# Kernel optimization log

Measured on AMD Instinct MI355X. Metric: run time of the kernel, lower is better.

Reference implementation:

```python
import jax, jax.numpy as jnp
import numpy as np

D_MODEL = 1024
NUM_HEADS = 16
DEPTH = D_MODEL // NUM_HEADS


def setup_inputs() -> dict:
    key = jax.random.key(0)
    ks = jax.random.split(key, 9)
    B, S = 2, 2048
    s = 1.0 / np.sqrt(D_MODEL)
    return {
        "x": jax.random.normal(ks[0], (B, S, D_MODEL), dtype=jnp.float32),
        "wq": jax.random.normal(ks[1], (D_MODEL, D_MODEL), dtype=jnp.float32) * s,
        "bq": jnp.zeros((D_MODEL,), dtype=jnp.float32),
        "wk": jax.random.normal(ks[2], (D_MODEL, D_MODEL), dtype=jnp.float32) * s,
        "bk": jnp.zeros((D_MODEL,), dtype=jnp.float32),
        "wv": jax.random.normal(ks[3], (D_MODEL, D_MODEL), dtype=jnp.float32) * s,
        "bv": jnp.zeros((D_MODEL,), dtype=jnp.float32),
        "wo": jax.random.normal(ks[4], (D_MODEL, D_MODEL), dtype=jnp.float32) * s,
        "bo": jnp.zeros((D_MODEL,), dtype=jnp.float32),
    }


def _split_heads(t):
    # [B, S, D] -> [B, H, S, depth]
    B, S, _ = t.shape
    return t.reshape(B, S, NUM_HEADS, DEPTH).transpose(0, 2, 1, 3)


def reference(x, wq, bq, wk, bk, wv, bv, wo, bo):
    B, S, _ = x.shape
    q = _split_heads(x @ wq + bq)
    k = _split_heads(x @ wk + bk)
    v = _split_heads(x @ wv + bv)
    scale = 1.0 / jnp.sqrt(jnp.asarray(DEPTH, dtype=x.dtype))
    logits = jnp.einsum("bhsd,bhtd->bhst", q, k) * scale  # [B,H,S,S]
    attn = jax.nn.softmax(logits, axis=-1)
    ctx = jnp.einsum("bhst,bhtd->bhsd", attn, v)  # [B,H,S,depth]
    concat = ctx.transpose(0, 2, 1, 3).reshape(B, S, D_MODEL)
    return concat @ wo + bo
```

## Files before the change

### kernel.cpp

```cpp
#include <hip/hip_runtime.h>
#include <hip/hip_bf16.h>

typedef __bf16 bf16;
typedef __bf16 bf16x4 __attribute__((ext_vector_type(4)));
typedef __bf16 bf16x8 __attribute__((ext_vector_type(8)));
typedef float f32x4 __attribute__((ext_vector_type(4)));

typedef __attribute__((address_space(3))) void lds_void;
typedef const __attribute__((address_space(1))) void gbl_void;

#define D_MODEL 1024
#define NHEAD 16
#define DEPTH 64
#define SEQ 2048
#define BATCH 2
#define NTOK (BATCH * SEQ)

#define Q_SCALE 0.18033688f

__global__ __launch_bounds__(256) void prep(const float* __restrict__ w0,
                                            const float* __restrict__ w1,
                                            const float* __restrict__ w2,
                                            const float* __restrict__ w3,
                                            const float* __restrict__ x,
                                            bf16* __restrict__ wtb,
                                            bf16* __restrict__ xb) {
    int z = blockIdx.z;
    int tx = threadIdx.x, ty = threadIdx.y;
    if (z < 4) {
        const float* w = (z == 0) ? w0 : (z == 1) ? w1 : (z == 2) ? w2 : w3;
        bf16* d = wtb + (size_t)z * D_MODEL * D_MODEL;
        __shared__ float tile[32][33];
        int c0 = blockIdx.x * 32;
        int r0 = blockIdx.y * 32;
#pragma unroll
        for (int i = 0; i < 4; i++)
            tile[ty + i * 8][tx] = w[(size_t)(r0 + ty + i * 8) * D_MODEL + c0 + tx];
        __syncthreads();
#pragma unroll
        for (int i = 0; i < 4; i++)
            d[(size_t)(c0 + ty + i * 8) * D_MODEL + r0 + tx] = (bf16)tile[tx][ty + i * 8];
    } else {
        int t = ty * 32 + tx;
        size_t i = ((size_t)(z - 4) * 1024 + blockIdx.y * 32 + blockIdx.x) * 256 + t;
        float4 v = ((const float4*)x)[i];
        bf16x4 o = {(bf16)v.x, (bf16)v.y, (bf16)v.z, (bf16)v.w};
        *(bf16x4*)&xb[i * 4] = o;
    }
}

__global__ __launch_bounds__(512, 2) void qkv_gemm(const bf16* __restrict__ xb,
                                                   const bf16* __restrict__ wtb,
                                                   const float* __restrict__ bq,
                                                   const float* __restrict__ bk,
                                                   const float* __restrict__ bv,
                                                   bf16* __restrict__ q,
                                                   bf16* __restrict__ k,
                                                   bf16* __restrict__ v) {
    __shared__ bf16 sm[65536];

    const int flat = blockIdx.x;
    const int wg = (flat & 7) * 24 + (flat >> 3);
    const int mt = wg & 15, nt = wg >> 4;
    const int row0 = mt << 8;
    const int z = nt >> 2;
    const int nb = (nt & 3) << 8;

    const int tid = threadIdx.x;
    const int lane = tid & 63, wave = tid >> 6;
    const int wm = wave >> 2, wn = wave & 3;
    const int quad = lane >> 4, l16 = lane & 15;
    const int kch = ((quad ^ ((l16 >> 1) & 3)) << 3);

    const int srow = lane >> 2;
    const int scg = (lane & 3) ^ ((lane >> 3) & 3);
    const int stDst = wave * 1024 + lane * 8;

    const bf16* Ag = xb + (size_t)(row0 + wave * 32 + srow) * D_MODEL + scg * 8;
    const bf16* Bg = wtb + (size_t)z * D_MODEL * D_MODEL
                   + (size_t)(nb + wave * 32 + srow) * D_MODEL + scg * 8;

    f32x4 acc[8][4] = {};
    bf16x8 bfr[4];

#define GLL(SRC, DST) __builtin_amdgcn_global_load_lds((gbl_void*)(SRC), (lds_void*)(DST), 16, 0, 0)
#define STG_A(T_, KQ_, BUF_) { \
    const bf16* s_ = Ag + (T_) * 64 + (KQ_) * 32; \
    bf16* d_ = sm + (BUF_) * 16384 + (KQ_) * 8192 + stDst; \
    GLL(s_, d_); GLL(s_ + 16 * D_MODEL, d_ + 512); }
#define STG_B(T_, KQ_, BUF_) { \
    const bf16* s_ = Bg + (T_) * 64 + (KQ_) * 32; \
    bf16* d_ = sm + 32768 + (BUF_) * 16384 + (KQ_) * 8192 + stDst; \
    GLL(s_, d_); GLL(s_ + 16 * D_MODEL, d_ + 512); }
#define WAIT6 { asm volatile("s_waitcnt vmcnt(6)" ::: "memory"); }
#define NOW

#define PHASE(BUF_, KQ_, MQ_, STG_STMT, WAIT_STMT) { \
    bf16x8 af[4]; \
    const int ab_ = (BUF_) * 16384 + (KQ_) * 8192 + (wm * 128 + (MQ_) * 64 + l16) * 32 + kch; \
    _Pragma("unroll") \
    for (int i_ = 0; i_ < 4; i_++) af[i_] = *(const bf16x8*)&sm[ab_ + i_ * 512]; \
    if ((MQ_) == 0) { \
        const int bb_ = 32768 + (BUF_) * 16384 + (KQ_) * 8192 + (wn * 64 + l16) * 32 + kch; \
        _Pragma("unroll") \
        for (int j_ = 0; j_ < 4; j_++) bfr[j_] = *(const bf16x8*)&sm[bb_ + j_ * 512]; \
    } \
    STG_STMT; \
    WAIT_STMT; \
    __builtin_amdgcn_sched_barrier(0); \
    __builtin_amdgcn_s_barrier(); \
    __builtin_amdgcn_s_setprio(1); \
    _Pragma("unroll") \
    for (int i_ = 0; i_ < 4; i_++) \
        _Pragma("unroll") \
        for (int j_ = 0; j_ < 4; j_++) \
            acc[(MQ_) * 4 + i_][j_] = __builtin_amdgcn_mfma_f32_16x16x32_bf16( \
                af[i_], bfr[j_], acc[(MQ_) * 4 + i_][j_], 0, 0, 0); \
    __builtin_amdgcn_s_setprio(0); \
    __builtin_amdgcn_sched_barrier(0); \
    __builtin_amdgcn_s_barrier(); }

    STG_B(0, 0, 0);
    STG_A(0, 0, 0);
    STG_B(0, 1, 0);
    STG_A(0, 1, 0);
    asm volatile("s_waitcnt vmcnt(4)" ::: "memory");
    STG_B(1, 0, 1);
    STG_A(1, 0, 1);
    STG_B(1, 1, 1);
    asm volatile("s_waitcnt vmcnt(6)" ::: "memory");
    __builtin_amdgcn_sched_barrier(0);
    __builtin_amdgcn_s_barrier();

#pragma unroll 1
    for (int it = 0; it < 8; ++it) {
        const int t1 = 2 * it + 1;
        const int t2 = (2 * it + 2) & 15;
        const int t3 = (2 * it + 3) & 15;
        PHASE(0, 0, 0, STG_A(t1, 1, 1), NOW)
        PHASE(0, 0, 1, STG_B(t2, 0, 0), NOW)
        PHASE(0, 1, 0, STG_A(t2, 0, 0), NOW)
        PHASE(0, 1, 1, STG_B(t2, 1, 0), WAIT6)
        PHASE(1, 0, 0, STG_A(t2, 1, 0), NOW)
        PHASE(1, 0, 1, STG_B(t3, 0, 1), NOW)
        PHASE(1, 1, 0, STG_A(t3, 0, 1), NOW)
        PHASE(1, 1, 1, STG_B(t3, 1, 1), WAIT6)
    }

#undef PHASE
#undef WAIT6
#undef NOW
#undef STG_A
#undef STG_B
#undef GLL

    const float* bias = (z == 0) ? bq : (z == 1) ? bk : bv;
    const int bI = row0 >> 11;
    const int sBase = row0 & 2047;
    if (z < 2) {
        bf16* dst = (z == 0) ? q : k;
        const float scl = (z == 0) ? Q_SCALE : 1.0f;
#pragma unroll
        for (int j = 0; j < 4; j++) {
            const int f = nb + wn * 64 + j * 16 + l16;
            const float bi = bias[f];
            const int hh = f >> 6, d = f & 63;
            bf16* dcol = dst + ((size_t)(bI * NHEAD + hh) * SEQ) * DEPTH + d;
#pragma unroll
            for (int mi = 0; mi < 8; mi++) {
                const int s0 = sBase + wm * 128 + (mi >> 2) * 64 + (mi & 3) * 16 + quad * 4;
#pragma unroll
                for (int r = 0; r < 4; r++)
                    dcol[(size_t)(s0 + r) * DEPTH] = (bf16)((acc[mi][j][r] + bi) * scl);
            }
        }
    } else {
#pragma unroll
        for (int j = 0; j < 4; j++) {
            const int f = nb + wn * 64 + j * 16 + l16;
            const float bi = bias[f];
            const int hh = f >> 6, d = f & 63;
            bf16* vrow = v + ((size_t)(bI * NHEAD + hh) * DEPTH + d) * SEQ;
#pragma unroll
            for (int mi = 0; mi < 8; mi++) {
                const int s0 = sBase + wm * 128 + (mi >> 2) * 64 + (mi & 3) * 16 + quad * 4;
                f32x4 a = acc[mi][j];
                bf16x4 ob = {(bf16)(a[0] + bi), (bf16)(a[1] + bi),
                             (bf16)(a[2] + bi), (bf16)(a[3] + bi)};
                *(bf16x4*)&vrow[s0] = ob;
            }
        }
    }
}

__global__ __launch_bounds__(256) void attn(const bf16* __restrict__ q,
                                            const bf16* __restrict__ k,
                                            const bf16* __restrict__ v,
                                            bf16* __restrict__ ctx) {
    __shared__ __align__(16) bf16 smb[32768];
    const int tid = threadIdx.x;
    const int lane = tid & 63, wave = tid >> 6;
    const int quad = lane >> 4, l16 = lane & 15;
    const int bh = blockIdx.x;
    const int q0 = blockIdx.y * 64;
    const size_t hb = (size_t)bh * SEQ * DEPTH;
    const bf16* qh = q + hb;
    const bf16* kh = k + hb;
    const bf16* vh = v + hb;

    bf16x8 bq_[4][2];
#pragma unroll
    for (int n = 0; n < 4; n++) {
        int qrow = q0 + n * 16 + l16;
#pragma unroll
        for (int c = 0; c < 2; c++)
            bq_[n][c] = *(const bf16x8*)&qh[(size_t)qrow * DEPTH + c * 32 + quad * 8];
    }

    f32x4 ov[4][4] = {};
    f32x4 lv = {};

    const int wb = wave * 8192;
    const int kchS = (lane & 7) ^ (((lane >> 3) & 3) << 1);
    const int vchS = (lane & 3) ^ ((lane >> 2) & 3);
    const int krdL = ((l16 >> 2) << 3) + (l16 & 3);
    const int ksw = ((l16 & 3) << 1) | ((l16 >> 2) & 1);
    const int vsw = (quad ^ (l16 & 3)) << 3;

#define GLL(SRC, DST) __builtin_amdgcn_global_load_lds((gbl_void*)(SRC), (lds_void*)(DST), 16, 0, 0)

#define STAGE(BUF_, T_) { \
    _Pragma("unroll") \
    for (int o_ = 0; o_ < 4; o_++) { \
        const bf16* s_ = kh + (size_t)((T_) + wave * 32 + o_ * 8 + (lane >> 3)) * DEPTH \
                       + ((kchS ^ (o_ & 1)) << 3); \
        GLL(s_, smb + wb + (BUF_) * 2048 + o_ * 512 + lane * 8); \
    } \
    _Pragma("unroll") \
    for (int o_ = 0; o_ < 4; o_++) { \
        const bf16* s_ = vh + (size_t)(o_ * 16 + (lane >> 2)) * SEQ + (T_) + wave * 32 \
                       + (vchS << 3); \
        GLL(s_, smb + wb + 4096 + (BUF_) * 2048 + o_ * 512 + lane * 8); \
    } }

#define COMPUTE(BUF_) { \
    f32x4 s[2][4] = {}; \
    __builtin_amdgcn_s_setprio(1); \
    _Pragma("unroll") \
    for (int c_ = 0; c_ < 2; c_++) \
        _Pragma("unroll") \
        for (int h_ = 0; h_ < 2; h_++) { \
            bf16x8 kf = *(const bf16x8*)&smb[wb + (BUF_) * 2048 + (krdL + h_ * 4) * 64 \
                                             + ((((c_ << 2) | quad) ^ ksw) << 3)]; \
            _Pragma("unroll") \
            for (int n_ = 0; n_ < 4; n_++) \
                s[h_][n_] = __builtin_amdgcn_mfma_f32_16x16x32_bf16(kf, bq_[n_][c_], s[h_][n_], 0, 0, 0); \
        } \
    __builtin_amdgcn_s_setprio(0); \
    bf16x8 pb[4]; \
    _Pragma("unroll") \
    for (int n_ = 0; n_ < 4; n_++) { \
        float e0 = __builtin_amdgcn_exp2f(s[0][n_][0]); \
        float e1 = __builtin_amdgcn_exp2f(s[0][n_][1]); \
        float e2 = __builtin_amdgcn_exp2f(s[0][n_][2]); \
        float e3 = __builtin_amdgcn_exp2f(s[0][n_][3]); \
        float e4 = __builtin_amdgcn_exp2f(s[1][n_][0]); \
        float e5 = __builtin_amdgcn_exp2f(s[1][n_][1]); \
        float e6 = __builtin_amdgcn_exp2f(s[1][n_][2]); \
        float e7 = __builtin_amdgcn_exp2f(s[1][n_][3]); \
        pb[n_][0] = (bf16)e0; pb[n_][1] = (bf16)e1; \
        pb[n_][2] = (bf16)e2; pb[n_][3] = (bf16)e3; \
        pb[n_][4] = (bf16)e4; pb[n_][5] = (bf16)e5; \
        pb[n_][6] = (bf16)e6; pb[n_][7] = (bf16)e7; \
        lv[n_] += ((e0 + e1) + (e2 + e3)) + ((e4 + e5) + (e6 + e7)); \
    } \
    __builtin_amdgcn_s_setprio(1); \
    _Pragma("unroll") \
    for (int t_ = 0; t_ < 4; t_++) { \
        bf16x8 vf = *(const bf16x8*)&smb[wb + 4096 + (BUF_) * 2048 + (t_ * 16 + l16) * 32 + vsw]; \
        _Pragma("unroll") \
        for (int n_ = 0; n_ < 4; n_++) \
            ov[t_][n_] = __builtin_amdgcn_mfma_f32_16x16x32_bf16(vf, pb[n_], ov[t_][n_], 0, 0, 0); \
    } \
    __builtin_amdgcn_s_setprio(0); }

#define WAITV(N_) { asm volatile("s_waitcnt vmcnt(" #N_ ")" ::: "memory"); }
#define SB0 __builtin_amdgcn_sched_barrier(0)

    const int tb = wave << 2;
    STAGE(0, ((tb) & 15) * 128);
#pragma unroll 1
    for (int i = 0; i < 16; i++) {
        if (i < 15) {
            STAGE((i + 1) & 1, ((tb + i + 1) & 15) * 128);
            WAITV(8);
        } else {
            WAITV(0);
        }
        SB0;
        COMPUTE(i & 1);
        SB0;
    }

#undef SB0
#undef WAITV
#undef COMPUTE
#undef STAGE
#undef GLL

    f32x4* Red  = (f32x4*)smb;
    f32x4* Lred = (f32x4*)((char*)smb + 32768);
    __syncthreads();
#pragma unroll
    for (int tt = 0; tt < 8; tt++)
        Red[(tt * 4 + wave) * 64 + lane] = ov[tt >> 2][tt & 3];
    Lred[wave * 64 + lane] = lv;
    __syncthreads();
    f32x4 ls = {};
#pragma unroll
    for (int w_ = 0; w_ < 4; w_++)
#pragma unroll
        for (int qd = 0; qd < 4; qd++)
            ls += Lred[w_ * 64 + qd * 16 + l16];
    const int b = bh >> 4, hh = bh & 15;
    const int wb1 = wave & 1;
#pragma unroll
    for (int u = 0; u < 2; u++) {
        int tt = wave * 2 + u;
        f32x4 sv = Red[(tt * 4 + 0) * 64 + lane] + Red[(tt * 4 + 1) * 64 + lane]
                 + Red[(tt * 4 + 2) * 64 + lane] + Red[(tt * 4 + 3) * 64 + lane];
        int n = wb1 * 2 + u, t = wave >> 1;
        float iv = 1.0f / (wb1 ? ls[2 + u] : ls[u]);
        bf16x4 ob = {(bf16)(sv[0] * iv), (bf16)(sv[1] * iv),
                     (bf16)(sv[2] * iv), (bf16)(sv[3] * iv)};
        size_t off = ((size_t)(b * SEQ + q0 + n * 16 + l16)) * D_MODEL
                   + hh * 64 + t * 16 + quad * 4;
        *(bf16x4*)&ctx[off] = ob;
    }
    __syncthreads();
#pragma unroll
    for (int tt = 8; tt < 16; tt++)
        Red[((tt - 8) * 4 + wave) * 64 + lane] = ov[tt >> 2][tt & 3];
    __syncthreads();
#pragma unroll
    for (int u = 0; u < 2; u++) {
        int rt = wave * 2 + u;
        f32x4 sv = Red[(rt * 4 + 0) * 64 + lane] + Red[(rt * 4 + 1) * 64 + lane]
                 + Red[(rt * 4 + 2) * 64 + lane] + Red[(rt * 4 + 3) * 64 + lane];
        int n = wb1 * 2 + u, t = 2 + (wave >> 1);
        float iv = 1.0f / (wb1 ? ls[2 + u] : ls[u]);
        bf16x4 ob = {(bf16)(sv[0] * iv), (bf16)(sv[1] * iv),
                     (bf16)(sv[2] * iv), (bf16)(sv[3] * iv)};
        size_t off = ((size_t)(b * SEQ + q0 + n * 16 + l16)) * D_MODEL
                   + hh * 64 + t * 16 + quad * 4;
        *(bf16x4*)&ctx[off] = ob;
    }
}

__global__ __launch_bounds__(256) void out_gemm(const bf16* __restrict__ ctx,
                                                const bf16* __restrict__ wot,
                                                const float* __restrict__ bo,
                                                float* __restrict__ out) {
    __shared__ bf16 As[64 * 32];
    __shared__ bf16 Bs[128 * 32];
    const int tid = threadIdx.x;
    const int lane = tid & 63, wave = tid >> 6;
    const int quad = lane >> 4, l16 = lane & 15;
    const int srow = lane >> 2, selem = (lane & 3) * 8;
    int row0 = blockIdx.y * 64, col0 = blockIdx.x * 128;
    f32x4 acc[4][2] = {};

    for (int k0 = 0; k0 < D_MODEL; k0 += 32) {
        __syncthreads();
        {
            const bf16* ga = ctx + (size_t)(row0 + wave * 16 + srow) * D_MODEL + k0 + selem;
            __builtin_amdgcn_global_load_lds((gbl_void*)ga, (lds_void*)(As + wave * 512 + lane * 8), 16, 0, 0);
        }
#pragma unroll
        for (int t = 0; t < 2; t++) {
            int m = wave * 2 + t;
            const bf16* gb = wot + (size_t)(col0 + m * 16 + srow) * D_MODEL + k0 + selem;
            __builtin_amdgcn_global_load_lds((gbl_void*)gb, (lds_void*)(Bs + m * 512 + lane * 8), 16, 0, 0);
        }
        __syncthreads();
        bf16x8 af[4], bfr[2];
#pragma unroll
        for (int i = 0; i < 4; i++)
            af[i] = *(const bf16x8*)&As[(i * 16 + l16) * 32 + quad * 8];
#pragma unroll
        for (int j = 0; j < 2; j++)
            bfr[j] = *(const bf16x8*)&Bs[(wave * 32 + j * 16 + l16) * 32 + quad * 8];
#pragma unroll
        for (int i = 0; i < 4; i++)
#pragma unroll
            for (int j = 0; j < 2; j++)
                acc[i][j] = __builtin_amdgcn_mfma_f32_16x16x32_bf16(af[i], bfr[j], acc[i][j], 0, 0, 0);
    }
#pragma unroll
    for (int i = 0; i < 4; i++)
#pragma unroll
        for (int j = 0; j < 2; j++) {
            int colg = col0 + wave * 32 + j * 16 + l16;
            float bi = bo[colg];
            int rbase = row0 + i * 16 + quad * 4;
#pragma unroll
            for (int r = 0; r < 4; r++)
                out[(size_t)(rbase + r) * D_MODEL + colg] = acc[i][j][r] + bi;
        }
}

extern "C" void kernel_launch(void* const* d_in, const int* in_sizes, int n_in,
                              void* d_out, int out_size, void* d_ws, size_t ws_size,
                              hipStream_t stream) {
    const float* x  = (const float*)d_in[0];
    const float* wq = (const float*)d_in[1];
    const float* bq = (const float*)d_in[2];
    const float* wk = (const float*)d_in[3];
    const float* bk = (const float*)d_in[4];
    const float* wv = (const float*)d_in[5];
    const float* bv = (const float*)d_in[6];
    const float* wo = (const float*)d_in[7];
    const float* bo = (const float*)d_in[8];
    float* out = (float*)d_out;

    const size_t MB = 1024 * 1024;
    char* ws = (char*)d_ws;
    bf16* xb  = (bf16*)(ws);
    bf16* wtb = (bf16*)(ws + 8 * MB);
    bf16* qb  = (bf16*)(ws + 16 * MB);
    bf16* kb  = (bf16*)(ws + 24 * MB);
    bf16* vb  = (bf16*)(ws + 32 * MB);
    bf16* ctx = (bf16*)(ws + 40 * MB);

    prep<<<dim3(32, 32, 8), dim3(32, 8), 0, stream>>>(wq, wk, wv, wo, x, wtb, xb);
    qkv_gemm<<<dim3(192), dim3(512), 0, stream>>>(xb, wtb, bq, bk, bv, qb, kb, vb);
    attn<<<dim3(BATCH * NHEAD, SEQ / 64), 256, 0, stream>>>(qb, kb, vb, ctx);
    out_gemm<<<dim3(8, 64), 256, 0, stream>>>(ctx, wtb + 3 * (size_t)D_MODEL * D_MODEL, bo, out);
}
```

Before: 191.1 us.

## Split attention block into 8 waves sharing K/V tiles across query groups

The attention kernel now launches 512 threads per block. Waves are split into 4 key-split groups times 2 query groups of 32 rows each. Only the first query group issues the global-to-LDS loads of K/V tiles, and both groups read the shared tiles, with block-wide barriers added around each compute step. The intent is more waves per CU and fewer accumulator registers per wave, which should improve latency hiding. The cost is two s_barriers per iteration and all waves walking through the K tiles in lockstep instead of staggered.

```diff
diff --git a/kernel.cpp b/kernel.cpp
--- a/kernel.cpp
+++ b/kernel.cpp
@@ -193,13 +193,14 @@
     }
 }
 
-__global__ __launch_bounds__(256) void attn(const bf16* __restrict__ q,
-                                            const bf16* __restrict__ k,
-                                            const bf16* __restrict__ v,
-                                            bf16* __restrict__ ctx) {
+__global__ __launch_bounds__(512, 4) void attn(const bf16* __restrict__ q,
+                                               const bf16* __restrict__ k,
+                                               const bf16* __restrict__ v,
+                                               bf16* __restrict__ ctx) {
     __shared__ __align__(16) bf16 smb[32768];
     const int tid = threadIdx.x;
     const int lane = tid & 63, wave = tid >> 6;
+    const int ks = wave & 3, qg = wave >> 2;
     const int quad = lane >> 4, l16 = lane & 15;
     const int bh = blockIdx.x;
     const int q0 = blockIdx.y * 64;
@@ -208,19 +209,19 @@
     const bf16* kh = k + hb;
     const bf16* vh = v + hb;
 
-    bf16x8 bq_[4][2];
-#pragma unroll
-    for (int n = 0; n < 4; n++) {
-        int qrow = q0 + n * 16 + l16;
+    bf16x8 bq_[2][2];
+#pragma unroll
+    for (int n = 0; n < 2; n++) {
+        int qrow = q0 + qg * 32 + n * 16 + l16;
 #pragma unroll
         for (int c = 0; c < 2; c++)
             bq_[n][c] = *(const bf16x8*)&qh[(size_t)qrow * DEPTH + c * 32 + quad * 8];
     }
 
-    f32x4 ov[4][4] = {};
-    f32x4 lv = {};
-
-    const int wb = wave * 8192;
+    f32x4 ov[4][2] = {};
+    float lvs[2] = {0.f, 0.f};
+
+    const int sb = ks * 8192;
     const int kchS = (lane & 7) ^ (((lane >> 3) & 3) << 1);
     const int vchS = (lane & 3) ^ ((lane >> 2) & 3);
     const int krdL = ((l16 >> 2) << 3) + (l16 & 3);
@@ -232,34 +233,34 @@
 #define STAGE(BUF_, T_) { \
     _Pragma("unroll") \
     for (int o_ = 0; o_ < 4; o_++) { \
-        const bf16* s_ = kh + (size_t)((T_) + wave * 32 + o_ * 8 + (lane >> 3)) * DEPTH \
+        const bf16* s_ = kh + (size_t)((T_) + ks * 32 + o_ * 8 + (lane >> 3)) * DEPTH \
                        + ((kchS ^ (o_ & 1)) << 3); \
-        GLL(s_, smb + wb + (BUF_) * 2048 + o_ * 512 + lane * 8); \
+        GLL(s_, smb + sb + (BUF_) * 2048 + o_ * 512 + lane * 8); \
     } \
     _Pragma("unroll") \
     for (int o_ = 0; o_ < 4; o_++) { \
-        const bf16* s_ = vh + (size_t)(o_ * 16 + (lane >> 2)) * SEQ + (T_) + wave * 32 \
+        const bf16* s_ = vh + (size_t)(o_ * 16 + (lane >> 2)) * SEQ + (T_) + ks * 32 \
                        + (vchS << 3); \
-        GLL(s_, smb + wb + 4096 + (BUF_) * 2048 + o_ * 512 + lane * 8); \
+        GLL(s_, smb + sb + 4096 + (BUF_) * 2048 + o_ * 512 + lane * 8); \
     } }
 
 #define COMPUTE(BUF_) { \
-    f32x4 s[2][4] = {}; \
+    f32x4 s[2][2] = {}; \
     __builtin_amdgcn_s_setprio(1); \
     _Pragma("unroll") \
     for (int c_ = 0; c_ < 2; c_++) \
         _Pragma("unroll") \
         for (int h_ = 0; h_ < 2; h_++) { \
-            bf16x8 kf = *(const bf16x8*)&smb[wb + (BUF_) * 2048 + (krdL + h_ * 4) * 64 \
+            bf16x8 kf = *(const bf16x8*)&smb[sb + (BUF_) * 2048 + (krdL + h_ * 4) * 64 \
                                              + ((((c_ << 2) | quad) ^ ksw) << 3)]; \
             _Pragma("unroll") \
-            for (int n_ = 0; n_ < 4; n_++) \
+            for (int n_ = 0; n_ < 2; n_++) \
                 s[h_][n_] = __builtin_amdgcn_mfma_f32_16x16x32_bf16(kf, bq_[n_][c_], s[h_][n_], 0, 0, 0); \
         } \
     __builtin_amdgcn_s_setprio(0); \
-    bf16x8 pb[4]; \
-    _Pragma("unroll") \
-    for (int n_ = 0; n_ < 4; n_++) { \
+    bf16x8 pb[2]; \
+    _Pragma("unroll") \
+    for (int n_ = 0; n_ < 2; n_++) { \
         float e0 = __builtin_amdgcn_exp2f(s[0][n_][0]); \
         float e1 = __builtin_amdgcn_exp2f(s[0][n_][1]); \
         float e2 = __builtin_amdgcn_exp2f(s[0][n_][2]); \
@@ -272,87 +273,97 @@
         pb[n_][2] = (bf16)e2; pb[n_][3] = (bf16)e3; \
         pb[n_][4] = (bf16)e4; pb[n_][5] = (bf16)e5; \
         pb[n_][6] = (bf16)e6; pb[n_][7] = (bf16)e7; \
-        lv[n_] += ((e0 + e1) + (e2 + e3)) + ((e4 + e5) + (e6 + e7)); \
+        lvs[n_] += ((e0 + e1) + (e2 + e3)) + ((e4 + e5) + (e6 + e7)); \
     } \
     __builtin_amdgcn_s_setprio(1); \
     _Pragma("unroll") \
     for (int t_ = 0; t_ < 4; t_++) { \
-        bf16x8 vf = *(const bf16x8*)&smb[wb + 4096 + (BUF_) * 2048 + (t_ * 16 + l16) * 32 + vsw]; \
+        bf16x8 vf = *(const bf16x8*)&smb[sb + 4096 + (BUF_) * 2048 + (t_ * 16 + l16) * 32 + vsw]; \
         _Pragma("unroll") \
-        for (int n_ = 0; n_ < 4; n_++) \
+        for (int n_ = 0; n_ < 2; n_++) \
             ov[t_][n_] = __builtin_amdgcn_mfma_f32_16x16x32_bf16(vf, pb[n_], ov[t_][n_], 0, 0, 0); \
     } \
     __builtin_amdgcn_s_setprio(0); }
 
-#define WAITV(N_) { asm volatile("s_waitcnt vmcnt(" #N_ ")" ::: "memory"); }
 #define SB0 __builtin_amdgcn_sched_barrier(0)
 
-    const int tb = wave << 2;
-    STAGE(0, ((tb) & 15) * 128);
+    if (qg == 0) STAGE(0, 0);
 #pragma unroll 1
     for (int i = 0; i < 16; i++) {
-        if (i < 15) {
-            STAGE((i + 1) & 1, ((tb + i + 1) & 15) * 128);
-            WAITV(8);
-        } else {
-            WAITV(0);
+        if (qg == 0) {
+            if (i < 15) {
+                STAGE((i + 1) & 1, (i + 1) * 128);
+                asm volatile("s_waitcnt vmcnt(8)" ::: "memory");
+            } else {
+                asm volatile("s_waitcnt vmcnt(0)" ::: "memory");
+            }
         }
         SB0;
+        __builtin_amdgcn_s_barrier();
         COMPUTE(i & 1);
         SB0;
+        __builtin_amdgcn_s_barrier();
     }
 
 #undef SB0
-#undef WAITV
 #undef COMPUTE
 #undef STAGE
 #undef GLL
 
     f32x4* Red  = (f32x4*)smb;
-    f32x4* Lred = (f32x4*)((char*)smb + 32768);
+    float* Lred = (float*)((char*)smb + 32768);
+    const int b = bh >> 4, hh = bh & 15;
+    const int tA = ks >> 1, nA = ks & 1;
+
     __syncthreads();
 #pragma unroll
-    for (int tt = 0; tt < 8; tt++)
-        Red[(tt * 4 + wave) * 64 + lane] = ov[tt >> 2][tt & 3];
-    Lred[wave * 64 + lane] = lv;
+    for (int t2 = 0; t2 < 2; t2++)
+#pragma unroll
+        for (int n = 0; n < 2; n++)
+            Red[((((qg * 2 + t2) * 2 + n) * 4) + ks) * 64 + lane] = ov[t2][n];
+#pragma unroll
+    for (int n = 0; n < 2; n++)
+        Lred[((qg * 2 + n) * 4 + ks) * 64 + lane] = lvs[n];
     __syncthreads();
-    f32x4 ls = {};
-#pragma unroll
-    for (int w_ = 0; w_ < 4; w_++)
-#pragma unroll
-        for (int qd = 0; qd < 4; qd++)
-            ls += Lred[w_ * 64 + qd * 16 + l16];
-    const int b = bh >> 4, hh = bh & 15;
-    const int wb1 = wave & 1;
-#pragma unroll
-    for (int u = 0; u < 2; u++) {
-        int tt = wave * 2 + u;
-        f32x4 sv = Red[(tt * 4 + 0) * 64 + lane] + Red[(tt * 4 + 1) * 64 + lane]
-                 + Red[(tt * 4 + 2) * 64 + lane] + Red[(tt * 4 + 3) * 64 + lane];
-        int n = wb1 * 2 + u, t = wave >> 1;
-        float iv = 1.0f / (wb1 ? ls[2 + u] : ls[u]);
+
+    float ls0 = 0.f, ls1 = 0.f;
+#pragma unroll
+    for (int k4 = 0; k4 < 4; k4++)
+#pragma unroll
+        for (int qd = 0; qd < 4; qd++) {
+            ls0 += Lred[((qg * 2 + 0) * 4 + k4) * 64 + qd * 16 + l16];
+            ls1 += Lred[((qg * 2 + 1) * 4 + k4) * 64 + qd * 16 + l16];
+        }
+    const float lsn = (ks & 1) ? ls1 : ls0;
+    const float iv = 1.0f / lsn;
+
+    {
+        f32x4 sv = Red[((((qg * 2 + tA) * 2 + nA) * 4) + 0) * 64 + lane]
+                 + Red[((((qg * 2 + tA) * 2 + nA) * 4) + 1) * 64 + lane]
+                 + Red[((((qg * 2 + tA) * 2 + nA) * 4) + 2) * 64 + lane]
+                 + Red[((((qg * 2 + tA) * 2 + nA) * 4) + 3) * 64 + lane];
         bf16x4 ob = {(bf16)(sv[0] * iv), (bf16)(sv[1] * iv),
                      (bf16)(sv[2] * iv), (bf16)(sv[3] * iv)};
-        size_t off = ((size_t)(b * SEQ + q0 + n * 16 + l16)) * D_MODEL
-                   + hh * 64 + t * 16 + quad * 4;
+        size_t off = ((size_t)(b * SEQ + q0 + qg * 32 + nA * 16 + l16)) * D_MODEL
+                   + hh * 64 + tA * 16 + quad * 4;
         *(bf16x4*)&ctx[off] = ob;
     }
     __syncthreads();
 #pragma unroll
-    for (int tt = 8; tt < 16; tt++)
-        Red[((tt - 8) * 4 + wave) * 64 + lane] = ov[tt >> 2][tt & 3];
+    for (int t2 = 0; t2 < 2; t2++)
+#pragma unroll
+        for (int n = 0; n < 2; n++)
+            Red[((((qg * 2 + t2) * 2 + n) * 4) + ks) * 64 + lane] = ov[2 + t2][n];
     __syncthreads();
-#pragma unroll
-    for (int u = 0; u < 2; u++) {
-        int rt = wave * 2 + u;
-        f32x4 sv = Red[(rt * 4 + 0) * 64 + lane] + Red[(rt * 4 + 1) * 64 + lane]
-                 + Red[(rt * 4 + 2) * 64 + lane] + Red[(rt * 4 + 3) * 64 + lane];
-        int n = wb1 * 2 + u, t = 2 + (wave >> 1);
-        float iv = 1.0f / (wb1 ? ls[2 + u] : ls[u]);
+    {
+        f32x4 sv = Red[((((qg * 2 + tA) * 2 + nA) * 4) + 0) * 64 + lane]
+                 + Red[((((qg * 2 + tA) * 2 + nA) * 4) + 1) * 64 + lane]
+                 + Red[((((qg * 2 + tA) * 2 + nA) * 4) + 2) * 64 + lane]
+                 + Red[((((qg * 2 + tA) * 2 + nA) * 4) + 3) * 64 + lane];
         bf16x4 ob = {(bf16)(sv[0] * iv), (bf16)(sv[1] * iv),
                      (bf16)(sv[2] * iv), (bf16)(sv[3] * iv)};
-        size_t off = ((size_t)(b * SEQ + q0 + n * 16 + l16)) * D_MODEL
-                   + hh * 64 + t * 16 + quad * 4;
+        size_t off = ((size_t)(b * SEQ + q0 + qg * 32 + nA * 16 + l16)) * D_MODEL
+                   + hh * 64 + (2 + tA) * 16 + quad * 4;
         *(bf16x4*)&ctx[off] = ob;
     }
 }
@@ -434,6 +445,6 @@
 
     prep<<<dim3(32, 32, 8), dim3(32, 8), 0, stream>>>(wq, wk, wv, wo, x, wtb, xb);
     qkv_gemm<<<dim3(192), dim3(512), 0, stream>>>(xb, wtb, bq, bk, bv, qb, kb, vb);
-    attn<<<dim3(BATCH * NHEAD, SEQ / 64), 256, 0, stream>>>(qb, kb, vb, ctx);
+    attn<<<dim3(BATCH * NHEAD, SEQ / 64), dim3(512), 0, stream>>>(qb, kb, vb, ctx);
     out_gemm<<<dim3(8, 64), 256, 0, stream>>>(ctx, wtb + 3 * (size_t)D_MODEL * D_MODEL, bo, out);
 }
```

Measured after the change: 191.0 us. About the same (-0.1%).
